# Performance work log

Hardware: AMD Instinct MI355X
Metric: run time of the kernel (lower is better)

## Reference

```python
import jax, jax.numpy as jnp
import numpy as np

E = 1024  # n_embd
L = 24    # n_layer
F = 4 * E # ffn hidden

def _ln(x, w, b):
    mu = jnp.mean(x)
    xm = x - mu
    var = jnp.mean(xm * xm)
    return xm * jax.lax.rsqrt(var + 1e-5) * w + b

def setup_inputs() -> dict:
    key = jax.random.key(0)
    ks = jax.random.split(key, 24)
    n = lambda k, s, sc=0.02: jax.random.normal(k, s, dtype=jnp.float32) * sc
    u = lambda k, s, lo, hi: jax.random.uniform(k, s, dtype=jnp.float32, minval=lo, maxval=hi)
    x = jax.random.normal(ks[0], (E,), dtype=jnp.float32)
    statea = jax.random.normal(ks[1], (L, E), dtype=jnp.float32)   # prev ln1 output
    stateb = n(ks[2], (L, E), 0.1)                                  # wkv numerator accum
    statec = u(ks[3], (L, E), 0.5, 1.5)                             # wkv denominator accum (>0)
    stated = jax.random.normal(ks[4], (L, E), dtype=jnp.float32)   # prev ln2 output
    state = jnp.stack([statea, stateb, statec, stated])
    return {
        "x": x,
        "state": state,
        "ln1w": 1.0 + n(ks[5], (L, E)),
        "ln1b": n(ks[6], (L, E)),
        "ln2w": 1.0 + n(ks[7], (L, E)),
        "ln2b": n(ks[8], (L, E)),
        "time_decay": u(ks[9], (L, E), 0.5, 0.99),   # module stores exp(raw) -> positive
        "time_first": u(ks[10], (L, E), 0.1, 1.0),   # module stores exp(raw) -> positive
        "key": n(ks[11], (L, 3, E, E)),              # stack([kk, vv, -rr]) per layer
        "outputv": n(ks[12], (L, E, E)),
        "mix_k": u(ks[13], (L, E), 0.0, 1.0),
        "mix_v": u(ks[14], (L, E), 0.0, 1.0),
        "mix_r": u(ks[15], (L, E), 0.0, 1.0),
        "mix_k_ffn": u(ks[16], (L, E), 0.0, 1.0),
        "mix_r_ffn": u(ks[17], (L, E), 0.0, 1.0),
        "key_ffn": n(ks[18], (L, F, E)),
        "receptance_ffn": n(ks[19], (L, E, E)),      # module stores -w; sign absorbed in init
        "value_ffn": n(ks[20], (L, E, F)),
    }

def reference(x, state, ln1w, ln1b, ln2w, ln2b, time_decay, time_first, key,
              outputv, mix_k, mix_v, mix_r, mix_k_ffn, mix_r_ffn,
              key_ffn, receptance_ffn, value_ffn):
    statea, stateb, statec, stated = state  # each [L, E]
    # forward pre-multiplies time-mix params by the per-layer OLD state (before the loop)
    kktk = mix_k * statea
    vvtv = mix_v * statea
    rrtr = mix_r * statea
    tmk = mix_k_ffn * stated
    tmr = mix_r_ffn * stated

    def step(cx, per):
        (l1w, l1b, l2w, l2b, td, tf, kw, ow, kk, vv, rr, tk, tr,
         kfw, rfw, vfw, sb, sc) = per
        # --- SA (time mixing / WKV state update) ---
        xn = _ln(cx, l1w, l1b)
        k = jnp.exp(kw[0] @ (xn + kk))
        v = kw[1] @ (xn + vv)
        r = jnp.exp(kw[2] @ (xn + rr)) + 1.0   # kw[2] = -rr weight
        wn = sb + tf * k * v
        d = sc * r + tf * k * r
        sx = cx + ow @ (wn / d)
        sb2 = sb * td + k * v
        sc2 = sc * td + k
        # --- FF (channel mixing) ---
        x2 = _ln(sx, l2w, l2b)
        kf = jnp.square(jax.nn.relu(kfw @ (x2 + tk)))
        rf = jnp.exp(rfw @ (x2 + tr))
        out = sx + (vfw @ kf) / (1.0 + rf)
        return out, (xn, sb2, sc2, x2)

    xs = (ln1w, ln1b, ln2w, ln2b, time_decay, time_first, key, outputv,
          kktk, vvtv, rrtr, tmk, tmr, key_ffn, receptance_ffn, value_ffn,
          stateb, statec)
    x_out, (sa, sb, sc, sd) = jax.lax.scan(step, x, xs)
    return x_out, jnp.stack([sa, sb, sc, sd])
```

## Files before the change

### kernel.cpp

```cpp
#include <hip/hip_runtime.h>

#define EDIM 1024
#define LNUM 24
#define FDIM 4096
#define NB 256
#define NT 512

__device__ __forceinline__ float wave_sum(float v) {
#pragma unroll
    for (int off = 32; off > 0; off >>= 1) v += __shfl_xor(v, off, 64);
    return v;
}

__device__ __forceinline__ float2 cload2(const float* p) {
    double d = __hip_atomic_load((const double*)p, __ATOMIC_RELAXED,
                                 __HIP_MEMORY_SCOPE_AGENT);
    float2 r;
    __builtin_memcpy(&r, &d, 8);
    return r;
}
__device__ __forceinline__ float cload1(const float* p) {
    return __hip_atomic_load(p, __ATOMIC_RELAXED, __HIP_MEMORY_SCOPE_AGENT);
}
__device__ __forceinline__ void cstore1(float* p, float v) {
    __hip_atomic_store(p, v, __ATOMIC_RELAXED, __HIP_MEMORY_SCOPE_AGENT);
}

#define FENCE()                                  \
    do {                                         \
        asm volatile("" ::: "memory");           \
        __builtin_amdgcn_sched_barrier(0);       \
    } while (0)

__device__ __forceinline__ void lbar() {
    asm volatile("s_waitcnt lgkmcnt(0)" ::: "memory");
    __builtin_amdgcn_sched_barrier(0);
    __builtin_amdgcn_s_barrier();
    asm volatile("" ::: "memory");
    __builtin_amdgcn_sched_barrier(0);
}

template <int P>
__device__ __forceinline__ void gbar(unsigned* grp, unsigned* flags, unsigned& bi) {
    asm volatile("s_waitcnt vmcnt(%0) lgkmcnt(0)" ::"i"(P) : "memory");
    __builtin_amdgcn_sched_barrier(0);
    __builtin_amdgcn_s_barrier();
    const unsigned bi1 = bi + 1u;
    if (threadIdx.x == 0) {
        const int g = blockIdx.x & 7;
        unsigned o = __hip_atomic_fetch_add(&grp[g << 4], 1u, __ATOMIC_RELAXED,
                                            __HIP_MEMORY_SCOPE_AGENT);
        if ((o & 31u) == 31u) {
            const unsigned tgt = 32u * bi1;
            int guard = 0;
            for (;;) {
                unsigned mn = 0xffffffffu;
#pragma unroll
                for (int i = 0; i < 8; ++i) {
                    unsigned v = __hip_atomic_load(&grp[i << 4], __ATOMIC_RELAXED,
                                                   __HIP_MEMORY_SCOPE_AGENT);
                    mn = (v < mn) ? v : mn;
                }
                if (mn >= tgt) break;
                __builtin_amdgcn_s_sleep(1);
                if (++guard > (1 << 20)) break;
            }
#pragma unroll 4
            for (int j = 0; j < 32; ++j)
                __hip_atomic_store(&flags[(g + 8 * j) << 4], bi1, __ATOMIC_RELAXED,
                                   __HIP_MEMORY_SCOPE_AGENT);
        } else {
            int guard = 0;
            while (__hip_atomic_load(&flags[blockIdx.x << 4], __ATOMIC_RELAXED,
                                     __HIP_MEMORY_SCOPE_AGENT) < bi1) {
                __builtin_amdgcn_s_sleep(1);
                if (++guard > (1 << 20)) break;
            }
        }
    }
    __builtin_amdgcn_s_barrier();
    asm volatile("" ::: "memory");
    __builtin_amdgcn_sched_barrier(0);
    ++bi;
}

__device__ __forceinline__ float dot16(const float4& p0, const float4& p1,
                                       const float4& p2, const float4& p3,
                                       const float4& a, const float4& b,
                                       const float4& c, const float4& d) {
    return p0.x * a.x + p0.y * a.y + p0.z * a.z + p0.w * a.w +
           p1.x * b.x + p1.y * b.y + p1.z * b.z + p1.w * b.w +
           p2.x * c.x + p2.y * c.y + p2.z * c.z + p2.w * c.w +
           p3.x * d.x + p3.y * d.y + p3.z * d.z + p3.w * d.w;
}

__device__ __forceinline__ float dot1024_pref(const float4& p0, const float4& p1,
                                              const float4& p2, const float4& p3,
                                              const float* op, int lane) {
    const float4* o = (const float4*)op;
    return wave_sum(dot16(p0, p1, p2, p3, o[lane], o[lane + 64], o[lane + 128],
                          o[lane + 192]));
}

__device__ __forceinline__ float dot512_pref(const float4& p0, const float4& p1,
                                             const float* op, int lane) {
    const float4* o = (const float4*)op;
    const float4 a = o[lane], b4 = o[lane + 64];
    return wave_sum(p0.x * a.x + p0.y * a.y + p0.z * a.z + p0.w * a.w +
                    p1.x * b4.x + p1.y * b4.y + p1.z * b4.z + p1.w * b4.w);
}

__global__ __launch_bounds__(NT, 2) void rwkv_persistent(
    const float* __restrict__ x_in, const float* __restrict__ state,
    const float* __restrict__ ln1w, const float* __restrict__ ln1b,
    const float* __restrict__ ln2w, const float* __restrict__ ln2b,
    const float* __restrict__ td, const float* __restrict__ tf,
    const float* __restrict__ key, const float* __restrict__ ow,
    const float* __restrict__ mixk, const float* __restrict__ mixv,
    const float* __restrict__ mixr, const float* __restrict__ mixkf,
    const float* __restrict__ mixrf, const float* __restrict__ kffn,
    const float* __restrict__ rffn, const float* __restrict__ vffn,
    float* __restrict__ out, float* __restrict__ ws, unsigned* __restrict__ grp,
    unsigned* __restrict__ flags) {
    __shared__ float smem[FDIM + 32];
    float* red = smem + FDIM;

    float* xbuf = ws;
    float* sxbuf = ws + 1024;
    float* kbuf = ws + 2048;
    float* vbuf = ws + 3072;
    float* rbuf = ws + 4096;
    float* kfbuf = ws + 5120;
    float* rdiv = ws + 9216;

    float* sa_out = out + EDIM;
    float* sb_out = sa_out + LNUM * EDIM;
    float* sc_out = sb_out + LNUM * EDIM;
    float* sd_out = sc_out + LNUM * EDIM;

    const int t = threadIdx.x;
    const int b = blockIdx.x;
    const int w = t >> 6;
    const int lane = t & 63;
    const int gw = (b << 3) + w;
    const int rrow = (b << 2) + (w >> 1);
    const int rh = w & 1;
    const int drow = (b << 2) + (w >> 2);
    const int dch = w & 3;
    unsigned bi = 0;

    float4 pA0, pA1, pA2, pA3, rA0, rA1;
    float4 pB0, pB1;
    float4 pC10, pC11, pC12, pC13, pC20, pC21, pC22, pC23, rC0, rC1;
    float4 pD0, pD1, pD2, pD3, pD4, pD5, pD6, pD7;

    {
        const float4* qA = (const float4*)(key + ((size_t)gw << 10));
        pA0 = qA[lane]; pA1 = qA[lane + 64]; pA2 = qA[lane + 128]; pA3 = qA[lane + 192];
        const float4* qR =
            (const float4*)(key + ((size_t)(2048 + rrow) << 10) + (rh << 9));
        rA0 = qR[lane]; rA1 = qR[lane + 64];
    }

    for (int l = 0; l < LNUM; ++l) {
        const float* cx = (l == 0) ? x_in : xbuf;
        const float* owl = ow + (size_t)l * EDIM * EDIM;
        const float* kfl = kffn + (size_t)l * FDIM * EDIM;
        const float* rfl = rffn + (size_t)l * EDIM * EDIM;
        const float* vfl = vffn + (size_t)l * EDIM * FDIM;
        const int le = l * EDIM;

        {
            const float2 xv = cload2(cx + 2 * t);
            float s = xv.x + xv.y, s2 = xv.x * xv.x + xv.y * xv.y;
#pragma unroll
            for (int off = 32; off > 0; off >>= 1) {
                s += __shfl_xor(s, off, 64);
                s2 += __shfl_xor(s2, off, 64);
            }
            if (lane == 0) { red[w] = s; red[8 + w] = s2; }
            lbar();
            float ts = 0.0f, ts2 = 0.0f;
#pragma unroll
            for (int i = 0; i < 8; ++i) { ts += red[i]; ts2 += red[8 + i]; }
            const float mu = ts * (1.0f / 1024.0f);
            const float inv = rsqrtf(ts2 * (1.0f / 1024.0f) - mu * mu + 1e-5f);
            const float2 wv = ((const float2*)(ln1w + le))[t];
            const float2 bv = ((const float2*)(ln1b + le))[t];
            const float2 xn = make_float2((xv.x - mu) * inv * wv.x + bv.x,
                                          (xv.y - mu) * inv * wv.y + bv.y);
            if (b == 0) ((float2*)(sa_out + le))[t] = xn;
            const float2 sav = ((const float2*)(state + le))[t];
            const float2 mk = ((const float2*)(mixk + le))[t];
            const float2 mv = ((const float2*)(mixv + le))[t];
            const float2 mr = ((const float2*)(mixr + le))[t];
            ((float2*)smem)[t] = make_float2(xn.x + mk.x * sav.x, xn.y + mk.y * sav.y);
            ((float2*)(smem + 1024))[t] =
                make_float2(xn.x + mv.x * sav.x, xn.y + mv.y * sav.y);
            ((float2*)(smem + 2048))[t] =
                make_float2(xn.x + mr.x * sav.x, xn.y + mr.y * sav.y);
            lbar();
            const int mat = gw >> 10;
            const float d1 = dot1024_pref(pA0, pA1, pA2, pA3, smem + (mat << 10), lane);
            if (lane == 0) {
                if (mat == 0) cstore1(kbuf + gw, expf(d1));
                else          cstore1(vbuf + gw - 1024, d1);
            }
            const float d2 = dot512_pref(rA0, rA1, smem + 2048 + (rh << 9), lane);
            if (lane == 0) red[16 + w] = d2;
            lbar();
            if (t < 4)
                cstore1(rbuf + (b << 2) + t,
                        expf(red[16 + 2 * t] + red[17 + 2 * t]) + 1.0f);
        }
        FENCE();
        {
            const float4* qB = (const float4*)(owl + ((size_t)rrow << 10) + (rh << 9));
            pB0 = qB[lane]; pB1 = qB[lane + 64];
            const float4* q1 = (const float4*)(kfl + ((size_t)gw << 10));
            pC10 = q1[lane]; pC11 = q1[lane + 64]; pC12 = q1[lane + 128]; pC13 = q1[lane + 192];
            const float4* q2 = (const float4*)(kfl + ((size_t)(gw + 2048) << 10));
            pC20 = q2[lane]; pC21 = q2[lane + 64]; pC22 = q2[lane + 128]; pC23 = q2[lane + 192];
            const float4* qR = (const float4*)(rfl + ((size_t)rrow << 10) + (rh << 9));
            rC0 = qR[lane]; rC1 = qR[lane + 64];
        }
        gbar<12>(grp, flags, bi);

        {
            const float2 k2 = cload2(kbuf + 2 * t);
            const float2 v2 = cload2(vbuf + 2 * t);
            const float2 r2 = cload2(rbuf + 2 * t);
            const float2 tf2 = ((const float2*)(tf + le))[t];
            const float2 sb2 = ((const float2*)(state + 1 * LNUM * EDIM + le))[t];
            const float2 sc2 = ((const float2*)(state + 2 * LNUM * EDIM + le))[t];
            const float g0 =
                (sb2.x + tf2.x * k2.x * v2.x) / (sc2.x * r2.x + tf2.x * k2.x * r2.x);
            const float g1 =
                (sb2.y + tf2.y * k2.y * v2.y) / (sc2.y * r2.y + tf2.y * k2.y * r2.y);
            ((float2*)smem)[t] = make_float2(g0, g1);
            if (b == 0) {
                const float2 td2 = ((const float2*)(td + le))[t];
                ((float2*)(sb_out + le))[t] =
                    make_float2(sb2.x * td2.x + k2.x * v2.x, sb2.y * td2.y + k2.y * v2.y);
                ((float2*)(sc_out + le))[t] =
                    make_float2(sc2.x * td2.x + k2.x, sc2.y * td2.y + k2.y);
            }
            lbar();
            const float pd = dot512_pref(pB0, pB1, smem + (rh << 9), lane);
            if (lane == 0) red[w] = pd;
            lbar();
            if (t < 4) {
                const int r = (b << 2) + t;
                cstore1(sxbuf + r, cload1(cx + r) + red[2 * t] + red[2 * t + 1]);
            }
        }
        FENCE();
        {
            const float4* q1 = (const float4*)(vfl + ((size_t)drow << 12) + (dch << 10));
            pD0 = q1[lane]; pD1 = q1[lane + 64]; pD2 = q1[lane + 128]; pD3 = q1[lane + 192];
            const float4* q2 =
                (const float4*)(vfl + ((size_t)(drow + 2) << 12) + (dch << 10));
            pD4 = q2[lane]; pD5 = q2[lane + 64]; pD6 = q2[lane + 128]; pD7 = q2[lane + 192];
        }
        gbar<8>(grp, flags, bi);

        {
            const float2 sxv = cload2(sxbuf + 2 * t);
            float s = sxv.x + sxv.y, s2 = sxv.x * sxv.x + sxv.y * sxv.y;
#pragma unroll
            for (int off = 32; off > 0; off >>= 1) {
                s += __shfl_xor(s, off, 64);
                s2 += __shfl_xor(s2, off, 64);
            }
            if (lane == 0) { red[w] = s; red[8 + w] = s2; }
            lbar();
            float ts = 0.0f, ts2 = 0.0f;
#pragma unroll
            for (int i = 0; i < 8; ++i) { ts += red[i]; ts2 += red[8 + i]; }
            const float mu = ts * (1.0f / 1024.0f);
            const float inv = rsqrtf(ts2 * (1.0f / 1024.0f) - mu * mu + 1e-5f);
            const float2 wv = ((const float2*)(ln2w + le))[t];
            const float2 bv = ((const float2*)(ln2b + le))[t];
            const float2 x2 = make_float2((sxv.x - mu) * inv * wv.x + bv.x,
                                          (sxv.y - mu) * inv * wv.y + bv.y);
            if (b == 0) ((float2*)(sd_out + le))[t] = x2;
            const float2 sdv = ((const float2*)(state + 3 * LNUM * EDIM + le))[t];
            const float2 mkf = ((const float2*)(mixkf + le))[t];
            const float2 mrf = ((const float2*)(mixrf + le))[t];
            ((float2*)smem)[t] = make_float2(x2.x + mkf.x * sdv.x, x2.y + mkf.y * sdv.y);
            ((float2*)(smem + 1024))[t] =
                make_float2(x2.x + mrf.x * sdv.x, x2.y + mrf.y * sdv.y);
            lbar();
            const float d1 = dot1024_pref(pC10, pC11, pC12, pC13, smem, lane);
            if (lane == 0) { const float rl = fmaxf(d1, 0.0f); cstore1(kfbuf + gw, rl * rl); }
            const float d2 = dot1024_pref(pC20, pC21, pC22, pC23, smem, lane);
            if (lane == 0) { const float rl = fmaxf(d2, 0.0f); cstore1(kfbuf + gw + 2048, rl * rl); }
            const float d3 = dot512_pref(rC0, rC1, smem + 1024 + (rh << 9), lane);
            if (lane == 0) red[16 + w] = d3;
            lbar();
            if (t < 4)
                cstore1(rdiv + (b << 2) + t,
                        1.0f / (1.0f + expf(red[16 + 2 * t] + red[17 + 2 * t])));
        }
        gbar<0>(grp, flags, bi);

        {
            const double* kfd = (const double*)kfbuf;
#pragma unroll
            for (int j = 0; j < 4; ++j)
                ((double*)smem)[t + j * 512] = __hip_atomic_load(
                    kfd + t + j * 512, __ATOMIC_RELAXED, __HIP_MEMORY_SCOPE_AGENT);
            lbar();
            const float pd0 = dot1024_pref(pD0, pD1, pD2, pD3, smem + (dch << 10), lane);
            const float pd1 = dot1024_pref(pD4, pD5, pD6, pD7, smem + (dch << 10), lane);
            if (lane == 0) { red[w] = pd0; red[8 + w] = pd1; }
            lbar();
            if (t < 4) {
                const int r = (b << 2) + t;
                const float dsum =
                    red[4 * t] + red[4 * t + 1] + red[4 * t + 2] + red[4 * t + 3];
                const float val = cload1(sxbuf + r) + dsum * cload1(rdiv + r);
                if (l == LNUM - 1) out[r] = val;
                else cstore1(xbuf + r, val);
            }
        }
        if (l < LNUM - 1) {
            FENCE();
            {
                const float* keyn = key + (size_t)(l + 1) * 3 * EDIM * EDIM;
                const float4* qA = (const float4*)(keyn + ((size_t)gw << 10));
                pA0 = qA[lane]; pA1 = qA[lane + 64]; pA2 = qA[lane + 128]; pA3 = qA[lane + 192];
                const float4* qR =
                    (const float4*)(keyn + ((size_t)(2048 + rrow) << 10) + (rh << 9));
                rA0 = qR[lane]; rA1 = qR[lane + 64];
            }
            gbar<6>(grp, flags, bi);
        }
    }
}

extern "C" void kernel_launch(void* const* d_in, const int* in_sizes, int n_in,
                              void* d_out, int out_size, void* d_ws, size_t ws_size,
                              hipStream_t stream) {
    const float* x_in = (const float*)d_in[0];
    const float* state = (const float*)d_in[1];
    const float* ln1w = (const float*)d_in[2];
    const float* ln1b = (const float*)d_in[3];
    const float* ln2w = (const float*)d_in[4];
    const float* ln2b = (const float*)d_in[5];
    const float* td = (const float*)d_in[6];
    const float* tf = (const float*)d_in[7];
    const float* key = (const float*)d_in[8];
    const float* ow = (const float*)d_in[9];
    const float* mixk = (const float*)d_in[10];
    const float* mixv = (const float*)d_in[11];
    const float* mixr = (const float*)d_in[12];
    const float* mixkf = (const float*)d_in[13];
    const float* mixrf = (const float*)d_in[14];
    const float* kffn = (const float*)d_in[15];
    const float* rffn = (const float*)d_in[16];
    const float* vffn = (const float*)d_in[17];

    float* out = (float*)d_out;
    float* ws = (float*)d_ws;

    unsigned* bar = (unsigned*)((char*)d_ws + 48 * 1024);
    unsigned* grp = bar;
    unsigned* flags = bar + 1024;

    hipMemsetAsync(bar, 0, 24 * 1024, stream);
    rwkv_persistent<<<NB, NT, 0, stream>>>(x_in, state, ln1w, ln1b, ln2w, ln2b, td, tf,
                                           key, ow, mixk, mixv, mixr, mixkf, mixrf,
                                           kffn, rffn, vffn, out, ws, grp, flags);
}
```

Before: 537.5 us.

## Rebalance weight prefetch across barriers and keep per-block partials in LDS

Moves the second key_ffn and receptance_ffn prefetches from the first barrier phase to the second, and the value_ffn prefetch to just before the FFN-output barrier. This spreads weight loads more evenly across the grid-barrier phases. The residual x, sx and the sigmoid divisor are now kept in shared memory instead of being written to and reloaded from global buffers, and only wave 0 waits on outstanding vector loads at a barrier. State-output writes are spread across different blocks per layer instead of always block 0. The risk is that the more complex barrier waits and LDS indexing are correct only if the prefetched registers and the red[] slots line up exactly.

```diff
diff --git a/kernel.cpp b/kernel.cpp
--- a/kernel.cpp
+++ b/kernel.cpp
@@ -19,17 +19,14 @@
     __builtin_memcpy(&r, &d, 8);
     return r;
 }
-__device__ __forceinline__ float cload1(const float* p) {
-    return __hip_atomic_load(p, __ATOMIC_RELAXED, __HIP_MEMORY_SCOPE_AGENT);
-}
 __device__ __forceinline__ void cstore1(float* p, float v) {
     __hip_atomic_store(p, v, __ATOMIC_RELAXED, __HIP_MEMORY_SCOPE_AGENT);
 }
 
-#define FENCE()                                  \
-    do {                                         \
-        asm volatile("" ::: "memory");           \
-        __builtin_amdgcn_sched_barrier(0);       \
+#define FENCE()                            \
+    do {                                   \
+        asm volatile("" ::: "memory");     \
+        __builtin_amdgcn_sched_barrier(0); \
     } while (0)
 
 __device__ __forceinline__ void lbar() {
@@ -41,8 +38,13 @@
 }
 
 template <int P>
-__device__ __forceinline__ void gbar(unsigned* grp, unsigned* flags, unsigned& bi) {
-    asm volatile("s_waitcnt vmcnt(%0) lgkmcnt(0)" ::"i"(P) : "memory");
+__device__ __forceinline__ void gbar(unsigned* grp, unsigned* flags, unsigned& bi,
+                                     int w) {
+    if (w == 0) {
+        asm volatile("s_waitcnt vmcnt(%0) lgkmcnt(0)" ::"i"(P) : "memory");
+    } else {
+        asm volatile("s_waitcnt lgkmcnt(0)" ::: "memory");
+    }
     __builtin_amdgcn_sched_barrier(0);
     __builtin_amdgcn_s_barrier();
     const unsigned bi1 = bi + 1u;
@@ -65,7 +67,7 @@
                 __builtin_amdgcn_s_sleep(1);
                 if (++guard > (1 << 20)) break;
             }
-#pragma unroll 4
+#pragma unroll 8
             for (int j = 0; j < 32; ++j)
                 __hip_atomic_store(&flags[(g + 8 * j) << 4], bi1, __ATOMIC_RELAXED,
                                    __HIP_MEMORY_SCOPE_AGENT);
@@ -122,16 +124,15 @@
     const float* __restrict__ rffn, const float* __restrict__ vffn,
     float* __restrict__ out, float* __restrict__ ws, unsigned* __restrict__ grp,
     unsigned* __restrict__ flags) {
-    __shared__ float smem[FDIM + 32];
+    __shared__ float smem[FDIM + 64];
     float* red = smem + FDIM;
 
-    float* xbuf = ws;
+    float* xnext = ws;
     float* sxbuf = ws + 1024;
     float* kbuf = ws + 2048;
     float* vbuf = ws + 3072;
     float* rbuf = ws + 4096;
     float* kfbuf = ws + 5120;
-    float* rdiv = ws + 9216;
 
     float* sa_out = out + EDIM;
     float* sb_out = sa_out + LNUM * EDIM;
@@ -143,10 +144,12 @@
     const int w = t >> 6;
     const int lane = t & 63;
     const int gw = (b << 3) + w;
+    const int mat = b >> 7;
     const int rrow = (b << 2) + (w >> 1);
     const int rh = w & 1;
     const int drow = (b << 2) + (w >> 2);
     const int dch = w & 3;
+    const bool slicer = ((t >> 1) == b);
     unsigned bi = 0;
 
     float4 pA0, pA1, pA2, pA3, rA0, rA1;
@@ -163,15 +166,20 @@
     }
 
     for (int l = 0; l < LNUM; ++l) {
-        const float* cx = (l == 0) ? x_in : xbuf;
         const float* owl = ow + (size_t)l * EDIM * EDIM;
         const float* kfl = kffn + (size_t)l * FDIM * EDIM;
         const float* rfl = rffn + (size_t)l * EDIM * EDIM;
         const float* vfl = vffn + (size_t)l * EDIM * FDIM;
         const int le = l * EDIM;
-
-        {
-            const float2 xv = cload2(cx + 2 * t);
+        const int bsel = (l << 2) & 255;
+
+        {
+            const float2 xv = (l == 0) ? ((const float2*)x_in)[t]
+                                       : cload2(xnext + 2 * t);
+            if (slicer) {
+                red[24 + ((t & 1) << 1)] = xv.x;
+                red[25 + ((t & 1) << 1)] = xv.y;
+            }
             float s = xv.x + xv.y, s2 = xv.x * xv.x + xv.y * xv.y;
 #pragma unroll
             for (int off = 32; off > 0; off >>= 1) {
@@ -189,7 +197,7 @@
             const float2 bv = ((const float2*)(ln1b + le))[t];
             const float2 xn = make_float2((xv.x - mu) * inv * wv.x + bv.x,
                                           (xv.y - mu) * inv * wv.y + bv.y);
-            if (b == 0) ((float2*)(sa_out + le))[t] = xn;
+            if (b == bsel) ((float2*)(sa_out + le))[t] = xn;
             const float2 sav = ((const float2*)(state + le))[t];
             const float2 mk = ((const float2*)(mixk + le))[t];
             const float2 mv = ((const float2*)(mixv + le))[t];
@@ -200,18 +208,21 @@
             ((float2*)(smem + 2048))[t] =
                 make_float2(xn.x + mr.x * sav.x, xn.y + mr.y * sav.y);
             lbar();
-            const int mat = gw >> 10;
             const float d1 = dot1024_pref(pA0, pA1, pA2, pA3, smem + (mat << 10), lane);
-            if (lane == 0) {
-                if (mat == 0) cstore1(kbuf + gw, expf(d1));
-                else          cstore1(vbuf + gw - 1024, d1);
-            }
             const float d2 = dot512_pref(rA0, rA1, smem + 2048 + (rh << 9), lane);
-            if (lane == 0) red[16 + w] = d2;
-            lbar();
-            if (t < 4)
-                cstore1(rbuf + (b << 2) + t,
-                        expf(red[16 + 2 * t] + red[17 + 2 * t]) + 1.0f);
+            if (lane == 0) { red[w] = d1; red[16 + w] = d2; }
+            lbar();
+            if (w == 0) {
+                if (lane < 8) {
+                    const float dv = red[lane];
+                    if (mat == 0) cstore1(kbuf + (b << 3) + lane, expf(dv));
+                    else          cstore1(vbuf + ((b - 128) << 3) + lane, dv);
+                } else if (lane < 12) {
+                    const int j = lane - 8;
+                    cstore1(rbuf + (b << 2) + j,
+                            expf(red[16 + 2 * j] + red[17 + 2 * j]) + 1.0f);
+                }
+            }
         }
         FENCE();
         {
@@ -219,12 +230,8 @@
             pB0 = qB[lane]; pB1 = qB[lane + 64];
             const float4* q1 = (const float4*)(kfl + ((size_t)gw << 10));
             pC10 = q1[lane]; pC11 = q1[lane + 64]; pC12 = q1[lane + 128]; pC13 = q1[lane + 192];
-            const float4* q2 = (const float4*)(kfl + ((size_t)(gw + 2048) << 10));
-            pC20 = q2[lane]; pC21 = q2[lane + 64]; pC22 = q2[lane + 128]; pC23 = q2[lane + 192];
-            const float4* qR = (const float4*)(rfl + ((size_t)rrow << 10) + (rh << 9));
-            rC0 = qR[lane]; rC1 = qR[lane + 64];
-        }
-        gbar<12>(grp, flags, bi);
+        }
+        gbar<6>(grp, flags, bi, w);
 
         {
             const float2 k2 = cload2(kbuf + 2 * t);
@@ -238,7 +245,7 @@
             const float g1 =
                 (sb2.y + tf2.y * k2.y * v2.y) / (sc2.y * r2.y + tf2.y * k2.y * r2.y);
             ((float2*)smem)[t] = make_float2(g0, g1);
-            if (b == 0) {
+            if (b == bsel + 1) {
                 const float2 td2 = ((const float2*)(td + le))[t];
                 ((float2*)(sb_out + le))[t] =
                     make_float2(sb2.x * td2.x + k2.x * v2.x, sb2.y * td2.y + k2.y * v2.y);
@@ -249,20 +256,20 @@
             const float pd = dot512_pref(pB0, pB1, smem + (rh << 9), lane);
             if (lane == 0) red[w] = pd;
             lbar();
-            if (t < 4) {
-                const int r = (b << 2) + t;
-                cstore1(sxbuf + r, cload1(cx + r) + red[2 * t] + red[2 * t + 1]);
+            if (w == 0 && lane < 4) {
+                const float sx = red[24 + lane] + red[2 * lane] + red[2 * lane + 1];
+                cstore1(sxbuf + (b << 2) + lane, sx);
+                red[28 + lane] = sx;
             }
         }
         FENCE();
         {
-            const float4* q1 = (const float4*)(vfl + ((size_t)drow << 12) + (dch << 10));
-            pD0 = q1[lane]; pD1 = q1[lane + 64]; pD2 = q1[lane + 128]; pD3 = q1[lane + 192];
-            const float4* q2 =
-                (const float4*)(vfl + ((size_t)(drow + 2) << 12) + (dch << 10));
-            pD4 = q2[lane]; pD5 = q2[lane + 64]; pD6 = q2[lane + 128]; pD7 = q2[lane + 192];
-        }
-        gbar<8>(grp, flags, bi);
+            const float4* q2 = (const float4*)(kfl + ((size_t)(gw + 2048) << 10));
+            pC20 = q2[lane]; pC21 = q2[lane + 64]; pC22 = q2[lane + 128]; pC23 = q2[lane + 192];
+            const float4* qR = (const float4*)(rfl + ((size_t)rrow << 10) + (rh << 9));
+            rC0 = qR[lane]; rC1 = qR[lane + 64];
+        }
+        gbar<6>(grp, flags, bi, w);
 
         {
             const float2 sxv = cload2(sxbuf + 2 * t);
@@ -283,7 +290,7 @@
             const float2 bv = ((const float2*)(ln2b + le))[t];
             const float2 x2 = make_float2((sxv.x - mu) * inv * wv.x + bv.x,
                                           (sxv.y - mu) * inv * wv.y + bv.y);
-            if (b == 0) ((float2*)(sd_out + le))[t] = x2;
+            if (b == bsel + 2) ((float2*)(sd_out + le))[t] = x2;
             const float2 sdv = ((const float2*)(state + 3 * LNUM * EDIM + le))[t];
             const float2 mkf = ((const float2*)(mixkf + le))[t];
             const float2 mrf = ((const float2*)(mixrf + le))[t];
@@ -292,17 +299,32 @@
                 make_float2(x2.x + mrf.x * sdv.x, x2.y + mrf.y * sdv.y);
             lbar();
             const float d1 = dot1024_pref(pC10, pC11, pC12, pC13, smem, lane);
-            if (lane == 0) { const float rl = fmaxf(d1, 0.0f); cstore1(kfbuf + gw, rl * rl); }
             const float d2 = dot1024_pref(pC20, pC21, pC22, pC23, smem, lane);
-            if (lane == 0) { const float rl = fmaxf(d2, 0.0f); cstore1(kfbuf + gw + 2048, rl * rl); }
             const float d3 = dot512_pref(rC0, rC1, smem + 1024 + (rh << 9), lane);
-            if (lane == 0) red[16 + w] = d3;
-            lbar();
-            if (t < 4)
-                cstore1(rdiv + (b << 2) + t,
-                        1.0f / (1.0f + expf(red[16 + 2 * t] + red[17 + 2 * t])));
-        }
-        gbar<0>(grp, flags, bi);
+            if (lane == 0) { red[w] = d1; red[8 + w] = d2; red[16 + w] = d3; }
+            lbar();
+            if (w == 0) {
+                if (lane < 8) {
+                    const float r1 = fmaxf(red[lane], 0.0f);
+                    const float r2 = fmaxf(red[8 + lane], 0.0f);
+                    cstore1(kfbuf + (b << 3) + lane, r1 * r1);
+                    cstore1(kfbuf + 2048 + (b << 3) + lane, r2 * r2);
+                } else if (lane < 12) {
+                    const int j = lane - 8;
+                    red[32 + j] =
+                        1.0f / (1.0f + expf(red[16 + 2 * j] + red[17 + 2 * j]));
+                }
+            }
+        }
+        FENCE();
+        {
+            const float4* q1 = (const float4*)(vfl + ((size_t)drow << 12) + (dch << 10));
+            pD0 = q1[lane]; pD1 = q1[lane + 64]; pD2 = q1[lane + 128]; pD3 = q1[lane + 192];
+            const float4* q2 =
+                (const float4*)(vfl + ((size_t)(drow + 2) << 12) + (dch << 10));
+            pD4 = q2[lane]; pD5 = q2[lane + 64]; pD6 = q2[lane + 128]; pD7 = q2[lane + 192];
+        }
+        gbar<8>(grp, flags, bi, w);
 
         {
             const double* kfd = (const double*)kfbuf;
@@ -315,13 +337,12 @@
             const float pd1 = dot1024_pref(pD4, pD5, pD6, pD7, smem + (dch << 10), lane);
             if (lane == 0) { red[w] = pd0; red[8 + w] = pd1; }
             lbar();
-            if (t < 4) {
-                const int r = (b << 2) + t;
-                const float dsum =
-                    red[4 * t] + red[4 * t + 1] + red[4 * t + 2] + red[4 * t + 3];
-                const float val = cload1(sxbuf + r) + dsum * cload1(rdiv + r);
-                if (l == LNUM - 1) out[r] = val;
-                else cstore1(xbuf + r, val);
+            if (w == 0 && lane < 4) {
+                const float ffn = red[4 * lane] + red[4 * lane + 1] +
+                                  red[4 * lane + 2] + red[4 * lane + 3];
+                const float val = red[28 + lane] + ffn * red[32 + lane];
+                if (l == LNUM - 1) out[(b << 2) + lane] = val;
+                else cstore1(xnext + (b << 2) + lane, val);
             }
         }
         if (l < LNUM - 1) {
@@ -334,7 +355,7 @@
                     (const float4*)(keyn + ((size_t)(2048 + rrow) << 10) + (rh << 9));
                 rA0 = qR[lane]; rA1 = qR[lane + 64];
             }
-            gbar<6>(grp, flags, bi);
+            gbar<6>(grp, flags, bi, w);
         }
     }
 }
```

Measured after the change: 501.3 us. -6.7%, faster.
